# Kernel tuning notes

Hardware: AMD Instinct MI355X
Metric: run time of the kernel (lower is better)

Reference implementation:

```python
import jax, jax.numpy as jnp
import numpy as np


def setup_inputs() -> dict:
    key = jax.random.key(0)
    k1, k2 = jax.random.split(key)
    B, T, D, P = 32, 8192, 128, 1024
    mel = jax.random.normal(k1, (B, T, D), dtype=jnp.float32)
    # durations in [0, 9); max possible sum = P*8 = T, so slices never overrun
    duration = jax.random.randint(k2, (B, P), 0, 9, dtype=jnp.int64)
    return {"mel": mel, "duration": duration}


def reference(mel, duration):
    # mel: (B, T, D) float; duration: (B, P) int, consumed sequentially.
    B, T, D = mel.shape
    P = duration.shape[1]
    ends = jnp.cumsum(duration, axis=1)  # (B, P): exclusive end frame of each phoneme
    t = jnp.arange(T)
    # segment id of frame t = first phoneme whose end > t; frames past sum(d) map to P
    seg = jax.vmap(lambda e: jnp.searchsorted(e, t, side="right"))(ends)  # (B, T)
    sums = jax.vmap(
        lambda m, s: jax.ops.segment_sum(m, s, num_segments=P + 1)
    )(mel, seg)[:, :P]  # (B, P, D), dropping the overflow bucket
    d = duration.astype(mel.dtype)[..., None]  # (B, P, 1)
    # mean over each phoneme's frames; zeros where duration == 0 (matches torch init)
    return jnp.where(d > 0, sums / jnp.maximum(d, 1), jnp.zeros((), mel.dtype))
```

## Files before the change

### kernel.cpp

```cpp
#include <hip/hip_runtime.h>

#define BB 32
#define TT 8192
#define DD 128
#define PP 1024

__global__ void phoneme_scan_kernel(const int* __restrict__ dur,
                                    int* __restrict__ starts) {
    __shared__ int sh[256];
    const int b = blockIdx.x;
    const int t = threadIdx.x;

    const int4 v = ((const int4*)(dur + b * PP))[t];
    const int local = v.x + v.y + v.z + v.w;

    sh[t] = local;
    __syncthreads();

    #pragma unroll
    for (int off = 1; off < 256; off <<= 1) {
        int other = (t >= off) ? sh[t - off] : 0;
        __syncthreads();
        sh[t] += other;
        __syncthreads();
    }
    const int excl = sh[t] - local;

    int4 s;
    s.x = excl;
    s.y = excl + v.x;
    s.z = excl + v.x + v.y;
    s.w = excl + v.x + v.y + v.z;
    ((int4*)(starts + b * PP))[t] = s;
}

__global__ void phoneme_avg_kernel(const float* __restrict__ mel,
                                   const int* __restrict__ dur,
                                   const int* __restrict__ starts,
                                   float* __restrict__ out) {
    const int row  = blockIdx.x * 8 + (threadIdx.x >> 5);
    const int lane = threadIdx.x & 31;
    const int b = row >> 10;

    const int d = dur[row];
    const int s = starts[row];

    const float4* base =
        (const float4*)(mel + ((size_t)b * TT + (size_t)s) * DD) + lane;

    float4 v[8];
    #pragma unroll
    for (int k = 0; k < 8; ++k) {
        v[k] = make_float4(0.f, 0.f, 0.f, 0.f);
        if (k < d) v[k] = base[k * (DD / 4)];
    }

    #pragma unroll
    for (int off = 4; off >= 1; off >>= 1) {
        #pragma unroll
        for (int k = 0; k < off; ++k) {
            v[k].x += v[k + off].x;
            v[k].y += v[k + off].y;
            v[k].z += v[k + off].z;
            v[k].w += v[k + off].w;
        }
    }

    const float inv = (d > 0) ? (1.0f / (float)d) : 0.0f;
    v[0].x *= inv; v[0].y *= inv; v[0].z *= inv; v[0].w *= inv;

    ((float4*)out)[(size_t)row * (DD / 4) + lane] = v[0];
}

extern "C" void kernel_launch(void* const* d_in, const int* in_sizes, int n_in,
                              void* d_out, int out_size, void* d_ws, size_t ws_size,
                              hipStream_t stream) {
    const float* mel = (const float*)d_in[0];
    const int*   dur = (const int*)d_in[1];
    float*       out = (float*)d_out;
    int*         starts = (int*)d_ws;

    phoneme_scan_kernel<<<BB, 256, 0, stream>>>(dur, starts);
    phoneme_avg_kernel<<<(BB * PP) / 8, 256, 0, stream>>>(mel, dur, starts, out);
}
```

Before: 182.6 us.

## Fuse duration prefix scan into averaging kernel with per-block recompute

Merges the separate scan kernel into the averaging kernel: each block recomputes its batch's prefix sum of durations in shared memory, then averages its 8 phoneme rows. This removes a kernel launch and the global round trip of start offsets. In exchange every block redoes the full 1024-element scan with several barriers before issuing its mel loads, adding latency and redundant work.

```diff
diff --git a/kernel.cpp b/kernel.cpp
--- a/kernel.cpp
+++ b/kernel.cpp
@@ -5,11 +5,16 @@
 #define DD 128
 #define PP 1024
 
-__global__ void phoneme_scan_kernel(const int* __restrict__ dur,
-                                    int* __restrict__ starts) {
+__global__ void __launch_bounds__(256)
+phoneme_fused_kernel(const float* __restrict__ mel,
+                     const int* __restrict__ dur,
+                     float* __restrict__ out) {
     __shared__ int sh[256];
-    const int b = blockIdx.x;
-    const int t = threadIdx.x;
+    __shared__ int starts_sh[PP];
+
+    const int b    = blockIdx.x >> 7;
+    const int pblk = blockIdx.x & 127;
+    const int t    = threadIdx.x;
 
     const int4 v = ((const int4*)(dur + b * PP))[t];
     const int local = v.x + v.y + v.z + v.w;
@@ -26,50 +31,44 @@
     }
     const int excl = sh[t] - local;
 
-    int4 s;
-    s.x = excl;
-    s.y = excl + v.x;
-    s.z = excl + v.x + v.y;
-    s.w = excl + v.x + v.y + v.z;
-    ((int4*)(starts + b * PP))[t] = s;
-}
+    starts_sh[4 * t + 0] = excl;
+    starts_sh[4 * t + 1] = excl + v.x;
+    starts_sh[4 * t + 2] = excl + v.x + v.y;
+    starts_sh[4 * t + 3] = excl + v.x + v.y + v.z;
+    __syncthreads();
 
-__global__ void phoneme_avg_kernel(const float* __restrict__ mel,
-                                   const int* __restrict__ dur,
-                                   const int* __restrict__ starts,
-                                   float* __restrict__ out) {
-    const int row  = blockIdx.x * 8 + (threadIdx.x >> 5);
-    const int lane = threadIdx.x & 31;
-    const int b = row >> 10;
+    const int r    = t >> 5;
+    const int lane = t & 31;
+    const int p    = pblk * 8 + r;
 
-    const int d = dur[row];
-    const int s = starts[row];
+    const int s = starts_sh[p];
+    const int d = dur[b * PP + p];
 
     const float4* base =
         (const float4*)(mel + ((size_t)b * TT + (size_t)s) * DD) + lane;
 
-    float4 v[8];
+    float4 acc[8];
     #pragma unroll
     for (int k = 0; k < 8; ++k) {
-        v[k] = make_float4(0.f, 0.f, 0.f, 0.f);
-        if (k < d) v[k] = base[k * (DD / 4)];
+        acc[k] = make_float4(0.f, 0.f, 0.f, 0.f);
+        if (k < d) acc[k] = base[k * (DD / 4)];
     }
 
     #pragma unroll
     for (int off = 4; off >= 1; off >>= 1) {
         #pragma unroll
         for (int k = 0; k < off; ++k) {
-            v[k].x += v[k + off].x;
-            v[k].y += v[k + off].y;
-            v[k].z += v[k + off].z;
-            v[k].w += v[k + off].w;
+            acc[k].x += acc[k + off].x;
+            acc[k].y += acc[k + off].y;
+            acc[k].z += acc[k + off].z;
+            acc[k].w += acc[k + off].w;
         }
     }
 
     const float inv = (d > 0) ? (1.0f / (float)d) : 0.0f;
-    v[0].x *= inv; v[0].y *= inv; v[0].z *= inv; v[0].w *= inv;
+    acc[0].x *= inv; acc[0].y *= inv; acc[0].z *= inv; acc[0].w *= inv;
 
-    ((float4*)out)[(size_t)row * (DD / 4) + lane] = v[0];
+    ((float4*)out)[((size_t)b * PP + p) * (DD / 4) + lane] = acc[0];
 }
 
 extern "C" void kernel_launch(void* const* d_in, const int* in_sizes, int n_in,
@@ -78,8 +77,6 @@
     const float* mel = (const float*)d_in[0];
     const int*   dur = (const int*)d_in[1];
     float*       out = (float*)d_out;
-    int*         starts = (int*)d_ws;
 
-    phoneme_scan_kernel<<<BB, 256, 0, stream>>>(dur, starts);
-    phoneme_avg_kernel<<<(BB * PP) / 8, 256, 0, stream>>>(mel, dur, starts, out);
+    phoneme_fused_kernel<<<(BB * PP) / 8, 256, 0, stream>>>(mel, dur, out);
 }
```

Result: no change. 180.1 us (-1.4%).
